# Optimization experiments

Measured on AMD Instinct MI355X. Metric: run time of the kernel, lower is better.

## Reference

```python
import jax, jax.numpy as jnp
import numpy as np

B, N, D = 1, 4096, 320
HEADS, DIM_HEAD = 8, 40
PHASE, Hm, Wm = 3, 64, 64  # guidance mask spatial dims; Hm*Wm == N


def setup_inputs() -> dict:
    key = jax.random.key(0)
    ks = jax.random.split(key, 7)
    s = 0.02
    x = jax.random.normal(ks[0], (B, N, D), jnp.float32)
    guidance_mask = jax.random.bernoulli(ks[1], 0.25, (B, PHASE, Hm, Wm)).astype(jnp.float32)
    Wq = jax.random.normal(ks[2], (D, HEADS * DIM_HEAD), jnp.float32) * s
    Wk = jax.random.normal(ks[3], (D, HEADS * DIM_HEAD), jnp.float32) * s
    Wv = jax.random.normal(ks[4], (D, HEADS * DIM_HEAD), jnp.float32) * s
    Wo = jax.random.normal(ks[5], (HEADS * DIM_HEAD, D), jnp.float32) * s
    bo = jnp.zeros((D,), jnp.float32)
    return {"x": x, "guidance_mask": guidance_mask, "Wq": Wq, "Wk": Wk,
            "Wv": Wv, "Wo": Wo, "bo": bo}


def reference(x, guidance_mask, Wq, Wk, Wv, Wo, bo):
    b, n, _ = x.shape
    h, dh = HEADS, DIM_HEAD
    scale = dh ** (-0.5)

    def split_heads(t):
        # b n (h d) -> (b h) n d
        return t.reshape(b, n, h, dh).transpose(0, 2, 1, 3).reshape(b * h, n, dh)

    q = split_heads(x @ Wq)
    k = split_heads(x @ Wk)
    v = split_heads(x @ Wv)

    sim = jnp.einsum('bid,bjd->bij', q, k) * scale  # (b*h, n, n)

    _, p, Hh, Ww = guidance_mask.shape
    HW = Hh * Ww  # == n
    g = guidance_mask.reshape(b, p, HW)
    # sum over phases of outer products, clamped at 1 (binary block mask)
    mask_sim = jnp.minimum(jnp.einsum('bpi,bpj->bij', g, g), 1.0)  # (b, HW, HW)
    mask_sim = jnp.repeat(mask_sim, h, axis=0)  # (b*h, HW, HW), heads within each b

    neg = -jnp.finfo(sim.dtype).max
    # original: sim[:, :, :HW][mask_sim == 0] = -max ; here n == HW so full matrix
    sim = jnp.where(mask_sim == 0, neg, sim)

    attn = jax.nn.softmax(sim, axis=-1)
    out = jnp.einsum('bij,bjd->bid', attn, v)  # (b*h, n, dh)
    out = out.reshape(b, h, n, dh).transpose(0, 2, 1, 3).reshape(b, n, h * dh)
    return out @ Wo + bo
```

## Files before the change

kernel.cpp:

```cpp
#include <hip/hip_runtime.h>
#include <hip/hip_bf16.h>
#include <stdint.h>

#define NT 4096
#define DM 320
#define NH 8
#define DH 40
#define KS 4
#define QSCALE 0.22811013f
#define PSTR 68
#define KFJB 640

typedef float f32x4 __attribute__((ext_vector_type(4)));
typedef __bf16 bf16x8 __attribute__((ext_vector_type(8)));

__device__ __forceinline__ unsigned short f2b(float f) {
  unsigned u = __builtin_bit_cast(unsigned, f);
  u += 0x7FFFu + ((u >> 16) & 1u);
  return (unsigned short)(u >> 16);
}

__device__ __forceinline__ bf16x8 ld_bf8(const unsigned short* p) {
  uint4 v = *(const uint4*)p;
  return __builtin_bit_cast(bf16x8, v);
}

__device__ __forceinline__ f32x4 mfma16(bf16x8 a, bf16x8 b, f32x4 c) {
  return __builtin_amdgcn_mfma_f32_16x16x32_bf16(a, b, c, 0, 0, 0);
}

__device__ __forceinline__ float fexp2(float x) {
#if __has_builtin(__builtin_amdgcn_exp2f)
  return __builtin_amdgcn_exp2f(x);
#else
  float r; asm("v_exp_f32 %0, %1" : "=v"(r) : "v"(x)); return r;
#endif
}

__device__ __forceinline__ uint2 pack4(float a, float b, float c, float d) {
  uint2 pk;
  pk.x = (unsigned)f2b(a) | ((unsigned)f2b(b) << 16);
  pk.y = (unsigned)f2b(c) | ((unsigned)f2b(d) << 16);
  return pk;
}

__device__ __forceinline__ size_t fmi(int tile, int nk, int k, int o) {
  return ((size_t)tile * nk + (k >> 5)) * 512 + (size_t)((k >> 3) & 3) * 128 +
         (size_t)(o & 15) * 8 + (k & 7);
}

__global__ __launch_bounds__(256) void prep_kernel(
    const float* __restrict__ x, const float* __restrict__ g,
    const float* __restrict__ Wq, const float* __restrict__ Wk,
    const float* __restrict__ Wv, const float* __restrict__ Wo,
    unsigned short* __restrict__ xbf, unsigned char* __restrict__ sigb,
    unsigned short* __restrict__ Wtf, int* __restrict__ perm,
    int* __restrict__ nqp) {
  const int b = blockIdx.x, t = threadIdx.x;
  if (b == 100) {
    __shared__ int cnt[256];
    unsigned char mys[16];
    int c1 = 0;
#pragma unroll
    for (int i = 0; i < 16; ++i) {
      int tok = t * 16 + i;
      unsigned s = 0;
      if (g[tok] != 0.f)          s |= 1u;
      if (g[NT + tok] != 0.f)     s |= 2u;
      if (g[2 * NT + tok] != 0.f) s |= 4u;
      sigb[tok] = (unsigned char)s;
      mys[i] = (unsigned char)s;
      c1 += (s != 0u);
    }
    cnt[t] = c1;
    __syncthreads();
    for (int off = 1; off < 256; off <<= 1) {
      int v = (t >= off) ? cnt[t - off] : 0;
      __syncthreads();
      cnt[t] += v;
      __syncthreads();
    }
    const int nq = cnt[255];
    int p1 = cnt[t] - c1;
    int p0 = nq + (t * 16 - p1);
#pragma unroll
    for (int i = 0; i < 16; ++i) {
      int tok = t * 16 + i;
      if (mys[i] != 0) perm[p1++] = tok;
      else             perm[p0++] = tok;
    }
    if (t == 0) nqp[0] = nq;
    return;
  }
  if (b > 100) {
    int base = (b - 101) * 2560;
#pragma unroll
    for (int j = 0; j < 10; ++j) {
      int i = (base + j * 256 + t) * 4;
      int m = i / DM, k = i % DM;
      float4 v = *(const float4*)(x + i);
      ushort4 u;
      u.x = f2b(v.x); u.y = f2b(v.y); u.z = f2b(v.z); u.w = f2b(v.w);
      *(ushort4*)(xbf + fmi(m >> 4, 10, k, m)) = u;
    }
    return;
  }
  __shared__ __align__(16) unsigned short lt[64 * 72];
  int kx = b % 5, cy = b / 5;
  int cm = cy % 5;
  const float* src;
  int rowbase;
  if (cy < 5)       { src = Wq; rowbase = cm * 64; }
  else if (cy < 10) { src = Wk; rowbase = 320 + cm * 64; }
  else if (cy < 15) { src = Wv; rowbase = 640 + cm * 64; }
  else              { src = Wo; rowbase = 960 + cm * 64; }
  const int c0 = cm * 64;
  const int k0 = kx * 64;
#pragma unroll
  for (int i = 0; i < 4; ++i) {
    int kr = (t >> 4) + i * 16, cc = (t & 15) * 4;
    float4 w4 = *(const float4*)&src[(size_t)(k0 + kr) * DM + c0 + cc];
    lt[(cc + 0) * 72 + kr] = f2b(w4.x);
    lt[(cc + 1) * 72 + kr] = f2b(w4.y);
    lt[(cc + 2) * 72 + kr] = f2b(w4.z);
    lt[(cc + 3) * 72 + kr] = f2b(w4.w);
  }
  __syncthreads();
#pragma unroll
  for (int i = 0; i < 2; ++i) {
    int idx = t + i * 256, cl = idx >> 3, ch = idx & 7;
    int c = rowbase + cl, k = k0 + ch * 8;
    *(uint4*)&Wtf[fmi(c >> 4, 10, k, c)] = *(const uint4*)&lt[cl * 72 + ch * 8];
  }
}

__global__ __launch_bounds__(256, 4) void qkv_gemm(
    const unsigned short* __restrict__ xbf, const unsigned short* __restrict__ Wtf,
    unsigned short* __restrict__ Qb, unsigned short* __restrict__ Kf,
    unsigned short* __restrict__ Vf) {
  const int t = threadIdx.x;
  const int w = t >> 6, lane = t & 63, quad = lane >> 4, ln = lane & 15;
  const int m0 = blockIdx.x * 64;
  const int cy = blockIdx.y;
  const int a = cy / 5;
  const int cc0 = (cy % 5) * 64;
  const int mt = (m0 >> 4) + w;
  const int ct0 = a * 20 + (cc0 >> 4);

  f32x4 acc[4] = {{0,0,0,0},{0,0,0,0},{0,0,0,0},{0,0,0,0}};
  for (int kc = 0; kc < 10; ++kc) {
    bf16x8 xf = ld_bf8(xbf + ((size_t)(mt * 10 + kc)) * 512 + lane * 8);
#pragma unroll
    for (int nt = 0; nt < 4; ++nt) {
      bf16x8 wf = ld_bf8(Wtf + ((size_t)((ct0 + nt) * 10 + kc)) * 512 + lane * 8);
      if (a < 2) acc[nt] = mfma16(wf, xf, acc[nt]);
      else       acc[nt] = mfma16(xf, wf, acc[nt]);
    }
  }
  if (a == 0) {
    const int m = m0 + w * 16 + ln;
#pragma unroll
    for (int nt = 0; nt < 4; ++nt) {
      int c = cc0 + nt * 16 + quad * 4;
      int h = c / DH, d = c % DH;
      uint2 pk = pack4(acc[nt][0] * QSCALE, acc[nt][1] * QSCALE,
                       acc[nt][2] * QSCALE, acc[nt][3] * QSCALE);
      *(uint2*)&Qb[((size_t)h * NT + m) * 64 + d] = pk;
    }
  } else if (a == 1) {
    const int m = m0 + w * 16 + ln;
#pragma unroll
    for (int nt = 0; nt < 4; ++nt) {
      int c = cc0 + nt * 16 + quad * 4;
      int h = c / DH, d = c % DH;
      uint2 pk = pack4(acc[nt][0], acc[nt][1], acc[nt][2], acc[nt][3]);
      size_t base = ((size_t)h * 256 + (m >> 4)) * KFJB;
      size_t idx = (d < 32)
          ? base + (size_t)(d >> 3) * 128 + (size_t)(m & 15) * 8 + (d & 7)
          : base + 512 + (size_t)(m & 15) * 8 + (d - 32);
      *(uint2*)&Kf[idx] = pk;
    }
  } else {
    const int mb = m0 + w * 16 + quad * 4;
#pragma unroll
    for (int nt = 0; nt < 4; ++nt) {
      int c = cc0 + nt * 16 + ln;
      int h = c / DH, d = c % DH;
      uint2 pk = pack4(acc[nt][0], acc[nt][1], acc[nt][2], acc[nt][3]);
      size_t idx = ((((((size_t)(h * 64 + (mb >> 6)) * 3 + (d >> 4)) * 2 +
                       ((mb >> 5) & 1)) * 4 + ((mb >> 3) & 3)) * 16 + (d & 15))) * 8 +
                   (mb & 7);
      *(uint2*)&Vf[idx] = pk;
    }
  }
}

__global__ __launch_bounds__(256, 4) void attn_kernel(
    const unsigned short* __restrict__ Qb, const unsigned short* __restrict__ Kf,
    const unsigned short* __restrict__ Vf, const unsigned char* __restrict__ sigb,
    const int* __restrict__ perm, const int* __restrict__ nqp,
    unsigned short* __restrict__ Opf, float* __restrict__ Lpart) {
  __shared__ __align__(16) unsigned short pt[4][32 * PSTR];
  const int t = threadIdx.x;
  const int w = t >> 6, lane = t & 63, quad = lane >> 4, ln = lane & 15;
  const int h = blockIdx.y, qt = blockIdx.x, sp = blockIdx.z;
  const int qrow = qt * 128 + w * 32;
  const int j0 = sp * 16;
  const int nq_pad = (nqp[0] + 127) & ~127;
  const bool writer = (qt * 128 >= nq_pad);

  const unsigned short* Kfh = Kf + (size_t)h * 256 * KFJB;
  const unsigned short* Vfh = Vf + (size_t)h * 196608;
  unsigned short* ptw = pt[w];
  const uint4 z4 = {0, 0, 0, 0};
  const uint4 ones4 = {0x3F803F80u, 0x3F803F80u, 0x3F803F80u, 0x3F803F80u};
  const bf16x8 onesb = __builtin_bit_cast(bf16x8, ones4);
  const bool vone = (ln == 8);

  bf16x8 qa[2][2];
  unsigned sqx4[2], uqx4[2];
  int morig[2];
  f32x4 o[3][2] = {{{0,0,0,0},{0,0,0,0}},{{0,0,0,0},{0,0,0,0}},{{0,0,0,0},{0,0,0,0}}};

#pragma unroll
  for (int tq = 0; tq < 2; ++tq) {
    int bp = qrow + tq * 16 + ln;
    int mo = perm[bp];
    morig[tq] = mo;
    if (!writer) {
      const unsigned short* Qp = Qb + ((size_t)h * NT + mo) * 64;
      qa[tq][0] = ld_bf8(Qp + quad * 8);
      uint4 q1 = z4;
      if (quad == 0) q1 = *(const uint4*)(Qp + 32);
      qa[tq][1] = __builtin_bit_cast(bf16x8, q1);
      unsigned s = sigb[mo];
      sqx4[tq] = s * 0x01010101u;
      uqx4[tq] = (s == 0u) ? 0xFFFFFFFFu : 0u;
      if (s == 0u) {
        qa[tq][0] = __builtin_bit_cast(bf16x8, z4);
        qa[tq][1] = __builtin_bit_cast(bf16x8, z4);
      }
    }
  }

  for (int jt = j0; jt < j0 + 16; ++jt) {
    if (!writer) {
      uint4 kfr0[4], kfr1[4];
#pragma unroll
      for (int nt = 0; nt < 4; ++nt) {
        const unsigned short* kb = Kfh + (size_t)(jt * 4 + nt) * KFJB;
        kfr0[nt] = *(const uint4*)(kb + lane * 8);
        kfr1[nt] = z4;
        if (lane < 16) kfr1[nt] = *(const uint4*)(kb + 512 + lane * 8);
      }
#pragma unroll
      for (int nt = 0; nt < 4; ++nt) {
        bf16x8 ka0 = __builtin_bit_cast(bf16x8, kfr0[nt]);
        bf16x8 ka1 = __builtin_bit_cast(bf16x8, kfr1[nt]);
        unsigned spj = *(const unsigned*)(sigb + jt * 64 + nt * 16 + quad * 4);
#pragma unroll
        for (int tq = 0; tq < 2; ++tq) {
          f32x4 acc = {0.f, 0.f, 0.f, 0.f};
          acc = mfma16(ka0, qa[tq][0], acc);
          acc = mfma16(ka1, qa[tq][1], acc);
          unsigned m4 = (spj & sqx4[tq]) | uqx4[tq];
          unsigned u[4];
#pragma unroll
          for (int r = 0; r < 4; ++r) {
            unsigned mb = (m4 >> (8 * r)) & 255u;
            float am = mb ? acc[r] : -3.0e38f;
            u[r] = __builtin_bit_cast(unsigned, fexp2(am));
          }
          uint2 pk;
          pk.x = (u[0] >> 16) | (u[1] & 0xffff0000u);
          pk.y = (u[2] >> 16) | (u[3] & 0xffff0000u);
          *(uint2*)&ptw[(tq * 16 + ln) * PSTR + nt * 16 + quad * 4] = pk;
        }
      }
    }
    uint4 vfr[6];
#pragma unroll
    for (int ot = 0; ot < 3; ++ot)
#pragma unroll
      for (int c = 0; c < 2; ++c)
        vfr[ot * 2 + c] =
            *(const uint4*)(Vfh + ((size_t)((jt * 3 + ot) * 2 + c)) * 512 + lane * 8);
    if (vone) { vfr[4] = ones4; vfr[5] = ones4; }

    bf16x8 pb[2][2];
    if (!writer) {
      asm volatile("s_waitcnt lgkmcnt(0)" ::: "memory");
#pragma unroll
      for (int tq = 0; tq < 2; ++tq) {
        pb[tq][0] = ld_bf8(&ptw[(tq * 16 + ln) * PSTR + quad * 8]);
        pb[tq][1] = ld_bf8(&ptw[(tq * 16 + ln) * PSTR + 32 + quad * 8]);
      }
    } else {
      pb[0][0] = onesb; pb[0][1] = onesb; pb[1][0] = onesb; pb[1][1] = onesb;
    }
#pragma unroll
    for (int ot = 0; ot < 3; ++ot) {
      bf16x8 va0 = __builtin_bit_cast(bf16x8, vfr[ot * 2]);
      bf16x8 va1 = __builtin_bit_cast(bf16x8, vfr[ot * 2 + 1]);
#pragma unroll
      for (int tq = 0; tq < 2; ++tq) {
        o[ot][tq] = mfma16(va0, pb[tq][0], o[ot][tq]);
        o[ot][tq] = mfma16(va1, pb[tq][1], o[ot][tq]);
      }
    }
  }

#pragma unroll
  for (int tq = 0; tq < 2; ++tq) {
    int m = morig[tq];
#pragma unroll
    for (int ot = 0; ot < 3; ++ot) {
      int d0 = ot * 16 + quad * 4;
      if (d0 < DH) {
        int c = h * DH + d0;
        uint2 pk = pack4(o[ot][tq][0], o[ot][tq][1], o[ot][tq][2], o[ot][tq][3]);
        *(uint2*)&Opf[fmi(sp * 256 + (m >> 4), 10, c, m)] = pk;
      }
    }
    if (quad == 2)
      Lpart[sp * NT + m] = o[2][tq][0];
  }
}

__global__ __launch_bounds__(256, 4) void out_gemm(
    const unsigned short* __restrict__ Opf, const float* __restrict__ Lpart,
    const unsigned short* __restrict__ Wtf, const float* __restrict__ bo,
    float* __restrict__ out) {
  const int t = threadIdx.x;
  const int w = t >> 6, lane = t & 63, quad = lane >> 4, ln = lane & 15;
  const int m0 = blockIdx.x * 64;
  const int cc0 = blockIdx.y * 64;
  const int mt = (m0 >> 4) + w;
  const int m = m0 + w * 16 + ln;
  const int ct0 = 60 + (cc0 >> 4);
  float ls = 0.f;
#pragma unroll
  for (int sp = 0; sp < KS; ++sp) ls += Lpart[sp * NT + m];
  const float inv = 1.f / ls;

  f32x4 acc[4] = {{0,0,0,0},{0,0,0,0},{0,0,0,0},{0,0,0,0}};
  for (int kc = 0; kc < 10; ++kc) {
    float s8[8] = {0, 0, 0, 0, 0, 0, 0, 0};
#pragma unroll
    for (int sp = 0; sp < KS; ++sp) {
      uint4 v = *(const uint4*)(Opf + ((size_t)((sp * 256 + mt) * 10 + kc)) * 512 +
                                lane * 8);
      unsigned vv[4] = {v.x, v.y, v.z, v.w};
#pragma unroll
      for (int j = 0; j < 4; ++j) {
        s8[2 * j]     += __builtin_bit_cast(float, vv[j] << 16);
        s8[2 * j + 1] += __builtin_bit_cast(float, vv[j] & 0xffff0000u);
      }
    }
    unsigned short af8[8];
#pragma unroll
    for (int j = 0; j < 8; ++j) af8[j] = f2b(s8[j] * inv);
    bf16x8 af = ld_bf8(af8);
#pragma unroll
    for (int nt = 0; nt < 4; ++nt) {
      bf16x8 wf = ld_bf8(Wtf + ((size_t)((ct0 + nt) * 10 + kc)) * 512 + lane * 8);
      acc[nt] = mfma16(wf, af, acc[nt]);
    }
  }
#pragma unroll
  for (int nt = 0; nt < 4; ++nt) {
    int c = cc0 + nt * 16 + quad * 4;
    float4 bv = *(const float4*)(bo + c);
    float4 ov;
    ov.x = acc[nt][0] + bv.x;
    ov.y = acc[nt][1] + bv.y;
    ov.z = acc[nt][2] + bv.z;
    ov.w = acc[nt][3] + bv.w;
    *(float4*)(out + (size_t)m * DM + c) = ov;
  }
}

extern "C" void kernel_launch(void* const* d_in, const int* in_sizes, int n_in,
                              void* d_out, int out_size, void* d_ws, size_t ws_size,
                              hipStream_t stream) {
  const float* x  = (const float*)d_in[0];
  const float* g  = (const float*)d_in[1];
  const float* Wq = (const float*)d_in[2];
  const float* Wk = (const float*)d_in[3];
  const float* Wv = (const float*)d_in[4];
  const float* Wo = (const float*)d_in[5];
  const float* bo = (const float*)d_in[6];
  float* out = (float*)d_out;

  char* ws = (char*)d_ws;
  const size_t SIG_OFF  = 0;
  const size_t NQ_OFF   = 4096;
  const size_t PERM_OFF = 8192;
  const size_t XBF_OFF  = 32768;
  const size_t WTF_OFF = XBF_OFF + (size_t)NT * DM * 2;
  const size_t QB_OFF  = WTF_OFF + (size_t)1280 * DM * 2;
  const size_t KF_OFF  = QB_OFF + (size_t)NH * NT * 64 * 2;
  const size_t VF_OFF  = KF_OFF + (size_t)NH * 256 * KFJB * 2;
  const size_t OPF_OFF = VF_OFF + (size_t)NH * 196608 * 2;
  const size_t LP_OFF  = OPF_OFF + (size_t)KS * 256 * 10 * 512 * 2;
  unsigned char* sigb  = (unsigned char*)(ws + SIG_OFF);
  int* nqp             = (int*)(ws + NQ_OFF);
  int* perm            = (int*)(ws + PERM_OFF);
  unsigned short* xbf  = (unsigned short*)(ws + XBF_OFF);
  unsigned short* Wtf  = (unsigned short*)(ws + WTF_OFF);
  unsigned short* Qb   = (unsigned short*)(ws + QB_OFF);
  unsigned short* Kf   = (unsigned short*)(ws + KF_OFF);
  unsigned short* Vf   = (unsigned short*)(ws + VF_OFF);
  unsigned short* Opf  = (unsigned short*)(ws + OPF_OFF);
  float* Lpart         = (float*)(ws + LP_OFF);

  prep_kernel<<<229, 256, 0, stream>>>(x, g, Wq, Wk, Wv, Wo, xbf, sigb, Wtf,
                                       perm, nqp);
  qkv_gemm<<<dim3(64, 15), 256, 0, stream>>>(xbf, Wtf, Qb, Kf, Vf);
  attn_kernel<<<dim3(32, NH, KS), 256, 0, stream>>>(Qb, Kf, Vf, sigb, perm, nqp,
                                                    Opf, Lpart);
  out_gemm<<<dim3(64, 5), 256, 0, stream>>>(Opf, Lpart, Wtf, bo, out);
}
```

Before: 147.3 us.

## Fuse bf16 prep into QKV and output GEMMs, split attention keys eight ways

```diff
diff --git a/kernel.cpp b/kernel.cpp
--- a/kernel.cpp
+++ b/kernel.cpp
@@ -6,7 +6,7 @@
 #define DM 320
 #define NH 8
 #define DH 40
-#define KS 4
+#define KS 8
 #define QSCALE 0.22811013f
 #define PSTR 68
 #define KFJB 640
@@ -49,15 +49,17 @@
          (size_t)(o & 15) * 8 + (k & 7);
 }
 
-__global__ __launch_bounds__(256) void prep_kernel(
+__global__ __launch_bounds__(256, 4) void qkv_gemm(
     const float* __restrict__ x, const float* __restrict__ g,
     const float* __restrict__ Wq, const float* __restrict__ Wk,
-    const float* __restrict__ Wv, const float* __restrict__ Wo,
-    unsigned short* __restrict__ xbf, unsigned char* __restrict__ sigb,
-    unsigned short* __restrict__ Wtf, int* __restrict__ perm,
-    int* __restrict__ nqp) {
-  const int b = blockIdx.x, t = threadIdx.x;
-  if (b == 100) {
+    const float* __restrict__ Wv,
+    unsigned char* __restrict__ sigb, int* __restrict__ perm,
+    int* __restrict__ nqp, unsigned short* __restrict__ Qb,
+    unsigned short* __restrict__ Kf, unsigned short* __restrict__ Vf) {
+  const int t = threadIdx.x;
+  const int cy = blockIdx.y;
+  if (cy == 15) {
+    if (blockIdx.x != 0) return;
     __shared__ int cnt[256];
     unsigned char mys[16];
     int c1 = 0;
@@ -92,67 +94,29 @@
     if (t == 0) nqp[0] = nq;
     return;
   }
-  if (b > 100) {
-    int base = (b - 101) * 2560;
-#pragma unroll
-    for (int j = 0; j < 10; ++j) {
-      int i = (base + j * 256 + t) * 4;
-      int m = i / DM, k = i % DM;
-      float4 v = *(const float4*)(x + i);
-      ushort4 u;
-      u.x = f2b(v.x); u.y = f2b(v.y); u.z = f2b(v.z); u.w = f2b(v.w);
-      *(ushort4*)(xbf + fmi(m >> 4, 10, k, m)) = u;
-    }
-    return;
-  }
-  __shared__ __align__(16) unsigned short lt[64 * 72];
-  int kx = b % 5, cy = b / 5;
-  int cm = cy % 5;
-  const float* src;
-  int rowbase;
-  if (cy < 5)       { src = Wq; rowbase = cm * 64; }
-  else if (cy < 10) { src = Wk; rowbase = 320 + cm * 64; }
-  else if (cy < 15) { src = Wv; rowbase = 640 + cm * 64; }
-  else              { src = Wo; rowbase = 960 + cm * 64; }
-  const int c0 = cm * 64;
-  const int k0 = kx * 64;
-#pragma unroll
-  for (int i = 0; i < 4; ++i) {
-    int kr = (t >> 4) + i * 16, cc = (t & 15) * 4;
-    float4 w4 = *(const float4*)&src[(size_t)(k0 + kr) * DM + c0 + cc];
-    lt[(cc + 0) * 72 + kr] = f2b(w4.x);
-    lt[(cc + 1) * 72 + kr] = f2b(w4.y);
-    lt[(cc + 2) * 72 + kr] = f2b(w4.z);
-    lt[(cc + 3) * 72 + kr] = f2b(w4.w);
-  }
-  __syncthreads();
-#pragma unroll
-  for (int i = 0; i < 2; ++i) {
-    int idx = t + i * 256, cl = idx >> 3, ch = idx & 7;
-    int c = rowbase + cl, k = k0 + ch * 8;
-    *(uint4*)&Wtf[fmi(c >> 4, 10, k, c)] = *(const uint4*)&lt[cl * 72 + ch * 8];
-  }
-}
-
-__global__ __launch_bounds__(256, 4) void qkv_gemm(
-    const unsigned short* __restrict__ xbf, const unsigned short* __restrict__ Wtf,
-    unsigned short* __restrict__ Qb, unsigned short* __restrict__ Kf,
-    unsigned short* __restrict__ Vf) {
-  const int t = threadIdx.x;
   const int w = t >> 6, lane = t & 63, quad = lane >> 4, ln = lane & 15;
   const int m0 = blockIdx.x * 64;
-  const int cy = blockIdx.y;
   const int a = cy / 5;
   const int cc0 = (cy % 5) * 64;
-  const int mt = (m0 >> 4) + w;
-  const int ct0 = a * 20 + (cc0 >> 4);
+  const float* Wsrc = (a == 0) ? Wq : ((a == 1) ? Wk : Wv);
+  const float* xrow = x + (size_t)(m0 + w * 16 + ln) * DM + quad * 8;
 
   f32x4 acc[4] = {{0,0,0,0},{0,0,0,0},{0,0,0,0},{0,0,0,0}};
   for (int kc = 0; kc < 10; ++kc) {
-    bf16x8 xf = ld_bf8(xbf + ((size_t)(mt * 10 + kc)) * 512 + lane * 8);
-#pragma unroll
-    for (int nt = 0; nt < 4; ++nt) {
-      bf16x8 wf = ld_bf8(Wtf + ((size_t)((ct0 + nt) * 10 + kc)) * 512 + lane * 8);
+    float4 a0 = *(const float4*)(xrow + kc * 32);
+    float4 a1 = *(const float4*)(xrow + kc * 32 + 4);
+    unsigned short x8[8];
+    x8[0] = f2b(a0.x); x8[1] = f2b(a0.y); x8[2] = f2b(a0.z); x8[3] = f2b(a0.w);
+    x8[4] = f2b(a1.x); x8[5] = f2b(a1.y); x8[6] = f2b(a1.z); x8[7] = f2b(a1.w);
+    bf16x8 xf = ld_bf8(x8);
+    const float* Wk0 = Wsrc + (size_t)(kc * 32 + quad * 8) * DM + cc0 + ln;
+#pragma unroll
+    for (int nt = 0; nt < 4; ++nt) {
+      const float* wp = Wk0 + nt * 16;
+      unsigned short w8[8];
+#pragma unroll
+      for (int e = 0; e < 8; ++e) w8[e] = f2b(wp[(size_t)e * DM]);
+      bf16x8 wf = ld_bf8(w8);
       if (a < 2) acc[nt] = mfma16(wf, xf, acc[nt]);
       else       acc[nt] = mfma16(xf, wf, acc[nt]);
     }
@@ -205,7 +169,7 @@
   const int w = t >> 6, lane = t & 63, quad = lane >> 4, ln = lane & 15;
   const int h = blockIdx.y, qt = blockIdx.x, sp = blockIdx.z;
   const int qrow = qt * 128 + w * 32;
-  const int j0 = sp * 16;
+  const int j0 = sp * 8;
   const int nq_pad = (nqp[0] + 127) & ~127;
   const bool writer = (qt * 128 >= nq_pad);
 
@@ -243,7 +207,7 @@
     }
   }
 
-  for (int jt = j0; jt < j0 + 16; ++jt) {
+  for (int jt = j0; jt < j0 + 8; ++jt) {
     if (!writer) {
       uint4 kfr0[4], kfr1[4];
 #pragma unroll
@@ -329,7 +293,7 @@
 
 __global__ __launch_bounds__(256, 4) void out_gemm(
     const unsigned short* __restrict__ Opf, const float* __restrict__ Lpart,
-    const unsigned short* __restrict__ Wtf, const float* __restrict__ bo,
+    const float* __restrict__ Wo, const float* __restrict__ bo,
     float* __restrict__ out) {
   const int t = threadIdx.x;
   const int w = t >> 6, lane = t & 63, quad = lane >> 4, ln = lane & 15;
@@ -337,7 +301,6 @@
   const int cc0 = blockIdx.y * 64;
   const int mt = (m0 >> 4) + w;
   const int m = m0 + w * 16 + ln;
-  const int ct0 = 60 + (cc0 >> 4);
   float ls = 0.f;
 #pragma unroll
   for (int sp = 0; sp < KS; ++sp) ls += Lpart[sp * NT + m];
@@ -361,9 +324,14 @@
 #pragma unroll
     for (int j = 0; j < 8; ++j) af8[j] = f2b(s8[j] * inv);
     bf16x8 af = ld_bf8(af8);
-#pragma unroll
-    for (int nt = 0; nt < 4; ++nt) {
-      bf16x8 wf = ld_bf8(Wtf + ((size_t)((ct0 + nt) * 10 + kc)) * 512 + lane * 8);
+    const float* Wk0 = Wo + (size_t)(kc * 32 + quad * 8) * DM + cc0 + ln;
+#pragma unroll
+    for (int nt = 0; nt < 4; ++nt) {
+      const float* wp = Wk0 + nt * 16;
+      unsigned short w8[8];
+#pragma unroll
+      for (int e = 0; e < 8; ++e) w8[e] = f2b(wp[(size_t)e * DM]);
+      bf16x8 wf = ld_bf8(w8);
       acc[nt] = mfma16(wf, af, acc[nt]);
     }
   }
@@ -396,9 +364,7 @@
   const size_t SIG_OFF  = 0;
   const size_t NQ_OFF   = 4096;
   const size_t PERM_OFF = 8192;
-  const size_t XBF_OFF  = 32768;
-  const size_t WTF_OFF = XBF_OFF + (size_t)NT * DM * 2;
-  const size_t QB_OFF  = WTF_OFF + (size_t)1280 * DM * 2;
+  const size_t QB_OFF   = 32768;
   const size_t KF_OFF  = QB_OFF + (size_t)NH * NT * 64 * 2;
   const size_t VF_OFF  = KF_OFF + (size_t)NH * 256 * KFJB * 2;
   const size_t OPF_OFF = VF_OFF + (size_t)NH * 196608 * 2;
@@ -406,18 +372,15 @@
   unsigned char* sigb  = (unsigned char*)(ws + SIG_OFF);
   int* nqp             = (int*)(ws + NQ_OFF);
   int* perm            = (int*)(ws + PERM_OFF);
-  unsigned short* xbf  = (unsigned short*)(ws + XBF_OFF);
-  unsigned short* Wtf  = (unsigned short*)(ws + WTF_OFF);
   unsigned short* Qb   = (unsigned short*)(ws + QB_OFF);
   unsigned short* Kf   = (unsigned short*)(ws + KF_OFF);
   unsigned short* Vf   = (unsigned short*)(ws + VF_OFF);
   unsigned short* Opf  = (unsigned short*)(ws + OPF_OFF);
   float* Lpart         = (float*)(ws + LP_OFF);
 
-  prep_kernel<<<229, 256, 0, stream>>>(x, g, Wq, Wk, Wv, Wo, xbf, sigb, Wtf,
-                                       perm, nqp);
-  qkv_gemm<<<dim3(64, 15), 256, 0, stream>>>(xbf, Wtf, Qb, Kf, Vf);
+  qkv_gemm<<<dim3(64, 16), 256, 0, stream>>>(x, g, Wq, Wk, Wv, sigb, perm, nqp,
+                                             Qb, Kf, Vf);
   attn_kernel<<<dim3(32, NH, KS), 256, 0, stream>>>(Qb, Kf, Vf, sigb, perm, nqp,
                                                     Opf, Lpart);
-  out_gemm<<<dim3(64, 5), 256, 0, stream>>>(Opf, Lpart, Wtf, bo, out);
-}
+  out_gemm<<<dim3(64, 5), 256, 0, stream>>>(Opf, Lpart, Wo, bo, out);
+}
```

Result: slower. 157.5 us (+6.9%).
